# Kernel optimization log

Hardware: AMD Instinct MI355X
Metric: run time of the kernel (lower is better)

The kernel has to match this reference:

```python
import jax, jax.numpy as jnp
import numpy as np

B, CL, QL, D = 32, 1024, 512, 256


def setup_inputs() -> dict:
    key = jax.random.key(0)
    ks = jax.random.split(key, 8)
    c = jax.random.normal(ks[0], (B, CL, D), jnp.float32)
    q = jax.random.normal(ks[1], (B, QL, D), jnp.float32)
    scale = 1.0 / np.sqrt(D)
    w_c = jax.random.normal(ks[2], (D,), jnp.float32) * scale
    b_c = jax.random.normal(ks[3], (), jnp.float32) * 0.01
    w_q = jax.random.normal(ks[4], (D,), jnp.float32) * scale
    b_q = jax.random.normal(ks[5], (), jnp.float32) * 0.01
    w_cq = jax.random.normal(ks[6], (D,), jnp.float32) * scale
    b_cq = jax.random.normal(ks[7], (), jnp.float32) * 0.01
    return {"c": c, "q": q, "w_c": w_c, "b_c": b_c, "w_q": w_q, "b_q": b_q,
            "w_cq": w_cq, "b_cq": b_cq}


def reference(c, q, w_c, b_c, w_q, b_q, w_cq, b_cq):
    # s[b,i,j] = w_c.c_i + w_q.q_j + w_cq.(c_i*q_j) + biases
    sc = c @ w_c + b_c                                   # (B, CL)
    sq = q @ w_q + b_q                                   # (B, QL)
    # The original per-j loop att_weight_cq(c * q_j) is a batched bilinear form.
    cq = jnp.einsum('bid,bjd,d->bij', c, q, w_cq) + b_cq  # (B, CL, QL)
    s = sc[:, :, None] + sq[:, None, :] + cq              # (B, CL, QL)
    a = jax.nn.softmax(s, axis=2)
    c2q_att = jnp.einsum('bij,bjd->bid', a, q)            # (B, CL, D)
    bvec = jax.nn.softmax(jnp.max(s, axis=2), axis=1)     # (B, CL)
    q2c = jnp.einsum('bi,bid->bd', bvec, c)               # (B, D)
    q2c_att = jnp.broadcast_to(q2c[:, None, :], c.shape)  # (B, CL, D)
    x = jnp.concatenate([c, c2q_att, c * c2q_att, c * q2c_att], axis=-1)
    return x
```

## Files before the change

### kernel.cpp

```cpp
#include <hip/hip_runtime.h>

#define B_  32
#define CL_ 1024
#define QL_ 512
#define D_  256

typedef _Float16 f16;
typedef __attribute__((ext_vector_type(2))) _Float16 f16x2;
typedef __attribute__((ext_vector_type(4))) _Float16 f16x4;
typedef __attribute__((ext_vector_type(8))) _Float16 f16x8;
typedef __attribute__((ext_vector_type(4))) float    f32x4;

__global__ __launch_bounds__(256) void k0_prep(const float* __restrict__ q,
                                               const float* __restrict__ w_q,
                                               f16* __restrict__ qF,
                                               f16* __restrict__ qTF,
                                               float* __restrict__ sqv) {
  __shared__ f16 q_l[64][258];
  int b = blockIdx.y, J = blockIdx.x, j0 = J * 64, tid = threadIdx.x;
  int r = tid >> 2, seg = tid & 3;
  const float* qrow = q + ((size_t)(b * QL_ + j0 + r)) * D_ + seg * 64;
  float dot = 0.f;
  #pragma unroll
  for (int u = 0; u < 16; ++u) {
    f32x4 v  = *(const f32x4*)(qrow + 4 * u);
    f32x4 wv = *(const f32x4*)(w_q + seg * 64 + 4 * u);
    f16x4 h;
    h[0] = (f16)v[0]; h[1] = (f16)v[1]; h[2] = (f16)v[2]; h[3] = (f16)v[3];
    *(f16x4*)(&q_l[r][seg * 64 + 4 * u]) = h;
    dot += v[0]*wv[0] + v[1]*wv[1] + v[2]*wv[2] + v[3]*wv[3];
  }
  dot += __shfl_xor(dot, 1, 64);
  dot += __shfl_xor(dot, 2, 64);
  if (seg == 0) sqv[b * QL_ + j0 + r] = dot;
  __syncthreads();

  const int ww = tid >> 6, l = tid & 63, g = l >> 4, l15 = l & 15;
  f16* qFb = qF + ((size_t)(b * 8 + J)) * 16384;
  #pragma unroll
  for (int t = 0; t < 8; ++t) {
    int task = ww * 8 + t;
    int dk = task >> 2, fj = task & 3;
    f16x8 v = *(const f16x8*)(&q_l[16 * fj + l15][dk * 32 + 8 * g]);
    *(f16x8*)(qFb + ((size_t)task * 64 + l) * 8) = v;
  }
  #pragma unroll
  for (int t = 0; t < 8; ++t) {
    int task = ww * 8 + t;
    int W = task >> 2, jtl = (task >> 1) & 1, fd = task & 1;
    f16x8 v;
    #pragma unroll
    for (int e = 0; e < 8; ++e)
      v[e] = q_l[32 * jtl + 8 * g + e][32 * W + 16 * fd + l15];
    *(f16x8*)(qTF + ((((size_t)(b * 8 + W) * 16 + (2 * J + jtl)) * 2 + fd) * 64 + l) * 8) = v;
  }
}

__global__ __launch_bounds__(512, 2) void k1_fused(
    const float* __restrict__ c, const f16* __restrict__ qF,
    const f16* __restrict__ qTF, const float* __restrict__ sqv,
    const float* __restrict__ w_c, const float* __restrict__ w_cq,
    float* __restrict__ out, float* __restrict__ mrow)
{
  __shared__ alignas(16) char smem[142848];
  f16 (*cw_t)[264]  = (f16 (*)[264])(smem);
  char* P_b         = smem;
  float (*o_l)[260] = (float (*)[260])(smem);
  float* sqv_l = (float*)(smem + 133120);
  float* wcq_l = (float*)(smem + 135168);
  float* wc_l  = (float*)(smem + 136192);
  float* scv_l = (float*)(smem + 137216);
  float (*red)[128] = (float (*)[128])(smem + 137728);
  float* mf = (float*)(smem + 141824);
  float* lf = (float*)(smem + 142336);

  const int tid = threadIdx.x;
  const int w = tid >> 6, l = tid & 63, g = l >> 4, l15 = l & 15;
  const int lin = blockIdx.x, xcd = lin & 7, slot = lin >> 3;
  const int b  = xcd * 4 + (slot >> 3);
  const int i0 = (slot & 7) * 128;

  if (tid < 256) { wcq_l[tid] = w_cq[tid]; wc_l[tid] = w_c[tid]; }
  sqv_l[tid] = sqv[b * QL_ + tid];
  __syncthreads();

  {
    int row = tid >> 2, seg = tid & 3;
    const float* crow = c + (size_t)(b * CL_ + i0 + row) * D_ + seg * 64;
    float dot = 0.f;
    #pragma unroll
    for (int u = 0; u < 16; ++u) {
      f32x4 v  = *(const f32x4*)(crow + 4 * u);
      f32x4 wv = *(const f32x4*)(wcq_l + seg * 64 + 4 * u);
      f32x4 w2 = *(const f32x4*)(wc_l  + seg * 64 + 4 * u);
      f16x4 h;
      h[0] = (f16)(v[0]*wv[0]); h[1] = (f16)(v[1]*wv[1]);
      h[2] = (f16)(v[2]*wv[2]); h[3] = (f16)(v[3]*wv[3]);
      *(f16x4*)(&cw_t[row][seg * 64 + 4 * u]) = h;
      dot += v[0]*w2[0] + v[1]*w2[1] + v[2]*w2[2] + v[3]*w2[3];
    }
    dot += __shfl_xor(dot, 1, 64); dot += __shfl_xor(dot, 2, 64);
    if (seg == 0) scv_l[row] = dot;
  }
  __syncthreads();

  f32x4 acc[8][4];
  #pragma unroll
  for (int fi = 0; fi < 8; ++fi)
    #pragma unroll
    for (int fj = 0; fj < 4; ++fj)
      acc[fi][fj] = (f32x4){0.f,0.f,0.f,0.f};

  const f16* qFb = qF + ((size_t)(b * 8 + w)) * 16384;
  #pragma unroll
  for (int dk = 0; dk < 8; ++dk) {
    f16x8 av[8];
    #pragma unroll
    for (int fi = 0; fi < 8; ++fi)
      av[fi] = *(const f16x8*)(&cw_t[16 * fi + l15][dk * 32 + 8 * g]);
    #pragma unroll
    for (int fj = 0; fj < 4; ++fj) {
      f16x8 bf = *(const f16x8*)(qFb + (((size_t)dk * 4 + fj) * 64 + l) * 8);
      #pragma unroll
      for (int fi = 0; fi < 8; ++fi)
        acc[fi][fj] = __builtin_amdgcn_mfma_f32_16x16x32_f16(av[fi], bf, acc[fi][fj], 0, 0, 0);
    }
  }

  #pragma unroll
  for (int fi = 0; fi < 8; ++fi) {
    #pragma unroll
    for (int r = 0; r < 4; ++r) {
      float mx = -1e30f;
      #pragma unroll
      for (int fj = 0; fj < 4; ++fj) {
        float v = acc[fi][fj][r] + sqv_l[64 * w + 16 * fj + l15];
        acc[fi][fj][r] = v;
        mx = fmaxf(mx, v);
      }
      mx = fmaxf(mx, __shfl_xor(mx, 1, 64));
      mx = fmaxf(mx, __shfl_xor(mx, 2, 64));
      mx = fmaxf(mx, __shfl_xor(mx, 4, 64));
      mx = fmaxf(mx, __shfl_xor(mx, 8, 64));
      if (l15 == 0) red[w][16 * fi + 4 * g + r] = mx;
    }
  }
  __syncthreads();
  if (tid < 128) {
    float m = red[0][tid];
    #pragma unroll
    for (int w2 = 1; w2 < 8; ++w2) m = fmaxf(m, red[w2][tid]);
    mf[tid] = m;
    mrow[b * CL_ + i0 + tid] = m + scv_l[tid];
  }
  __syncthreads();
  #pragma unroll
  for (int fi = 0; fi < 8; ++fi) {
    #pragma unroll
    for (int r = 0; r < 4; ++r) {
      float mv = mf[16 * fi + 4 * g + r];
      float s = 0.f;
      #pragma unroll
      for (int fj = 0; fj < 4; ++fj) {
        float p = __expf(acc[fi][fj][r] - mv);
        acc[fi][fj][r] = p;
        s += p;
      }
      s += __shfl_xor(s, 1, 64); s += __shfl_xor(s, 2, 64);
      s += __shfl_xor(s, 4, 64); s += __shfl_xor(s, 8, 64);
      if (l15 == 0) red[w][16 * fi + 4 * g + r] = s;
    }
  }
  __syncthreads();
  if (tid < 128) {
    float s = 0.f;
    #pragma unroll
    for (int w2 = 0; w2 < 8; ++w2) s += red[w2][tid];
    lf[tid] = 1.0f / s;
  }
  __syncthreads();

  #pragma unroll
  for (int fi = 0; fi < 8; ++fi) {
    #pragma unroll
    for (int r = 0; r < 4; ++r) {
      int row = 16 * fi + 4 * g + r;
      float inv = lf[row];
      #pragma unroll
      for (int fj = 0; fj < 4; ++fj) {
        *(f16*)(P_b + (((row << 10) + 128 * w + 32 * fj + 2 * l15) ^ ((row & 7) << 4)))
            = (f16)(acc[fi][fj][r] * inv);
      }
    }
  }
  __syncthreads();

  f32x4 o[8][2];
  #pragma unroll
  for (int fi = 0; fi < 8; ++fi) { o[fi][0] = (f32x4){0.f,0.f,0.f,0.f}; o[fi][1] = o[fi][0]; }
  const f16* qTFb = qTF + ((size_t)(b * 8 + w)) * 16384;
  #pragma unroll
  for (int jt = 0; jt < 16; ++jt) {
    f16x8 qf0 = *(const f16x8*)(qTFb + (((size_t)jt * 2 + 0) * 64 + l) * 8);
    f16x8 qf1 = *(const f16x8*)(qTFb + (((size_t)jt * 2 + 1) * 64 + l) * 8);
    #pragma unroll
    for (int fi = 0; fi < 8; ++fi) {
      int row = 16 * fi + l15;
      f16x8 pa = *(const f16x8*)(P_b + (((row << 10) + 64 * jt + 16 * g) ^ ((row & 7) << 4)));
      o[fi][0] = __builtin_amdgcn_mfma_f32_16x16x32_f16(pa, qf0, o[fi][0], 0, 0, 0);
      o[fi][1] = __builtin_amdgcn_mfma_f32_16x16x32_f16(pa, qf1, o[fi][1], 0, 0, 0);
    }
  }
  __syncthreads();

  #pragma unroll
  for (int fi = 0; fi < 8; ++fi)
    #pragma unroll
    for (int fd = 0; fd < 2; ++fd)
      #pragma unroll
      for (int r = 0; r < 4; ++r)
        o_l[16 * fi + 4 * g + r][32 * w + 16 * fd + l15] = o[fi][fd][r];
  __syncthreads();

  #pragma unroll
  for (int s = 0; s < 16; ++s) {
    int idx = tid + 512 * s;
    int row = idx >> 6, c4 = (idx & 63) * 4;
    size_t rowoff = (size_t)(b * CL_ + i0 + row);
    f32x4 c2q = *(const f32x4*)(&o_l[row][c4]);
    f32x4 cv  = *(const f32x4*)(c + rowoff * D_ + c4);
    f32x4 prod;
    prod[0] = cv[0]*c2q[0]; prod[1] = cv[1]*c2q[1];
    prod[2] = cv[2]*c2q[2]; prod[3] = cv[3]*c2q[3];
    float* ob = out + rowoff * (4 * D_) + c4;
    *(f32x4*)(ob)          = cv;
    *(f32x4*)(ob + D_)     = c2q;
    *(f32x4*)(ob + 2 * D_) = prod;
  }
}

__global__ __launch_bounds__(256) void k2a_bvec(const float* __restrict__ mrow,
                                                float* __restrict__ bvec) {
  __shared__ float red[256];
  int b = blockIdx.x, tid = threadIdx.x;
  f32x4 v = *(const f32x4*)(mrow + b * CL_ + tid * 4);
  float mx = fmaxf(fmaxf(v[0], v[1]), fmaxf(v[2], v[3]));
  red[tid] = mx;
  __syncthreads();
  for (int s = 128; s > 0; s >>= 1) {
    if (tid < s) red[tid] = fmaxf(red[tid], red[tid + s]);
    __syncthreads();
  }
  float gmx = red[0];
  __syncthreads();
  f32x4 e;
  e[0] = __expf(v[0] - gmx); e[1] = __expf(v[1] - gmx);
  e[2] = __expf(v[2] - gmx); e[3] = __expf(v[3] - gmx);
  red[tid] = e[0] + e[1] + e[2] + e[3];
  __syncthreads();
  for (int s = 128; s > 0; s >>= 1) {
    if (tid < s) red[tid] += red[tid + s];
    __syncthreads();
  }
  float inv = 1.0f / red[0];
  e[0] *= inv; e[1] *= inv; e[2] *= inv; e[3] *= inv;
  *(f32x4*)(bvec + b * CL_ + tid * 4) = e;
}

__global__ __launch_bounds__(256) void k2b_part(const float* __restrict__ c,
                                                const float* __restrict__ bvec,
                                                float* __restrict__ part) {
  __shared__ f32x4 pl[4][64];
  int ch = blockIdx.x, b = blockIdx.y, tid = threadIdx.x;
  int ro = tid >> 6, dl = tid & 63;
  const float* cb = c + ((size_t)b * CL_ + ch * 128) * D_;
  const float* bv = bvec + b * CL_ + ch * 128;
  f32x4 acc = (f32x4){0.f, 0.f, 0.f, 0.f};
  for (int i = ro; i < 128; i += 4) {
    float wgt = bv[i];
    f32x4 v = *(const f32x4*)(cb + (size_t)i * D_ + dl * 4);
    acc[0] += wgt * v[0]; acc[1] += wgt * v[1];
    acc[2] += wgt * v[2]; acc[3] += wgt * v[3];
  }
  pl[ro][dl] = acc;
  __syncthreads();
  if (tid < 64) {
    f32x4 s = (pl[0][tid] + pl[1][tid]) + (pl[2][tid] + pl[3][tid]);
    *(f32x4*)(part + ((size_t)(b * 8 + ch)) * D_ + tid * 4) = s;
  }
}

__global__ __launch_bounds__(256) void k2c_red(const float* __restrict__ part,
                                               float* __restrict__ q2c) {
  int b = blockIdx.x, d = threadIdx.x;
  float s = 0.f;
  #pragma unroll
  for (int ch = 0; ch < 8; ++ch) s += part[((size_t)(b * 8 + ch)) * D_ + d];
  q2c[b * D_ + d] = s;
}

__global__ __launch_bounds__(256) void k3_tail(const float* __restrict__ c,
                                               const float* __restrict__ q2c,
                                               float* __restrict__ out) {
  size_t idx = (size_t)blockIdx.x * 256 + threadIdx.x;
  int b   = (int)(idx >> 16);
  int rem = (int)(idx & 65535);
  int i = rem >> 6, d4 = (rem & 63) * 4;
  f32x4 cv = *(const f32x4*)(c + (size_t)(b * CL_ + i) * D_ + d4);
  f32x4 gv = *(const f32x4*)(q2c + b * D_ + d4);
  f32x4 r;
  r[0] = cv[0]*gv[0]; r[1] = cv[1]*gv[1]; r[2] = cv[2]*gv[2]; r[3] = cv[3]*gv[3];
  *(f32x4*)(out + (size_t)(b * CL_ + i) * (4 * D_) + 3 * D_ + d4) = r;
}

extern "C" void kernel_launch(void* const* d_in, const int* in_sizes, int n_in,
                              void* d_out, int out_size, void* d_ws, size_t ws_size,
                              hipStream_t stream) {
  const float* c    = (const float*)d_in[0];
  const float* q    = (const float*)d_in[1];
  const float* w_c  = (const float*)d_in[2];
  const float* w_q  = (const float*)d_in[4];
  const float* w_cq = (const float*)d_in[6];
  float* out = (float*)d_out;
  char* ws = (char*)d_ws;
  f16*   qF   = (f16*)ws;
  f16*   qTF  = (f16*)(ws + 8388608);
  float* sqv  = (float*)(ws + 16777216);
  float* mrow = (float*)(ws + 16842752);
  float* bvec = (float*)(ws + 16973824);
  float* part = (float*)(ws + 17104896);
  float* q2c  = (float*)(ws + 17367040);

  hipLaunchKernelGGL(k0_prep,  dim3(8, 32),  dim3(256), 0, stream,
                     q, w_q, qF, qTF, sqv);
  hipLaunchKernelGGL(k1_fused, dim3(256),    dim3(512), 0, stream,
                     c, qF, qTF, sqv, w_c, w_cq, out, mrow);
  hipLaunchKernelGGL(k2a_bvec, dim3(32),     dim3(256), 0, stream, mrow, bvec);
  hipLaunchKernelGGL(k2b_part, dim3(8, 32),  dim3(256), 0, stream, c, bvec, part);
  hipLaunchKernelGGL(k2c_red,  dim3(32),     dim3(256), 0, stream, part, q2c);
  hipLaunchKernelGGL(k3_tail,  dim3(8192),   dim3(256), 0, stream, c, q2c, out);
}
```

Baseline: 95.09 us.

## Split c*w_cq prep into separate kernel and halve k1 row tile for occupancy

Moves the c*w_cq fp16 conversion and c·w_c dot product out of the fused attention kernel into a new prep kernel. That kernel writes MFMA-fragment-ordered fp16 data and scv to workspace. The fused kernel now processes 64 rows per block instead of 128, using about half the LDS and fewer accumulators, and launches 512 blocks with a higher occupancy hint. The aim is better latency hiding and more parallelism. The cost is an extra kernel launch, an extra global round trip for the cwF intermediate, and reloading q fragments twice as often across blocks.

```diff
diff --git a/kernel.cpp b/kernel.cpp
--- a/kernel.cpp
+++ b/kernel.cpp
@@ -56,79 +56,93 @@
   }
 }
 
-__global__ __launch_bounds__(512, 2) void k1_fused(
-    const float* __restrict__ c, const f16* __restrict__ qF,
+__global__ __launch_bounds__(256) void k0c_cw(const float* __restrict__ c,
+                                              const float* __restrict__ w_c,
+                                              const float* __restrict__ w_cq,
+                                              f16* __restrict__ cwF,
+                                              float* __restrict__ scv_ws) {
+  __shared__ f16 cw_l[64][264];
+  int T = blockIdx.x, b = blockIdx.y, tid = threadIdx.x;
+  int i0 = T * 64;
+  int row = tid >> 2, seg = tid & 3;
+  const float* crow = c + (size_t)(b * CL_ + i0 + row) * D_ + seg * 64;
+  float dot = 0.f;
+  #pragma unroll
+  for (int u = 0; u < 16; ++u) {
+    f32x4 v  = *(const f32x4*)(crow + 4 * u);
+    f32x4 wv = *(const f32x4*)(w_cq + seg * 64 + 4 * u);
+    f32x4 w2 = *(const f32x4*)(w_c  + seg * 64 + 4 * u);
+    f16x4 h;
+    h[0] = (f16)(v[0]*wv[0]); h[1] = (f16)(v[1]*wv[1]);
+    h[2] = (f16)(v[2]*wv[2]); h[3] = (f16)(v[3]*wv[3]);
+    *(f16x4*)(&cw_l[row][seg * 64 + 4 * u]) = h;
+    dot += v[0]*w2[0] + v[1]*w2[1] + v[2]*w2[2] + v[3]*w2[3];
+  }
+  dot += __shfl_xor(dot, 1, 64); dot += __shfl_xor(dot, 2, 64);
+  if (seg == 0) scv_ws[b * CL_ + i0 + row] = dot;
+  __syncthreads();
+
+  const int ww = tid >> 6, l = tid & 63, g = l >> 4, l15 = l & 15;
+  f16* dst = cwF + ((size_t)(b * 16 + T)) * 32 * 512;
+  #pragma unroll
+  for (int t = 0; t < 8; ++t) {
+    int task = ww * 8 + t;
+    int fi = task >> 3, dk = task & 7;
+    f16x8 v = *(const f16x8*)(&cw_l[16 * fi + l15][dk * 32 + 8 * g]);
+    *(f16x8*)(dst + ((size_t)task * 64 + l) * 8) = v;
+  }
+}
+
+__global__ __launch_bounds__(512, 4) void k1_fused(
+    const f16* __restrict__ cwF, const f16* __restrict__ qF,
     const f16* __restrict__ qTF, const float* __restrict__ sqv,
-    const float* __restrict__ w_c, const float* __restrict__ w_cq,
+    const float* __restrict__ scv_ws, const float* __restrict__ c,
     float* __restrict__ out, float* __restrict__ mrow)
 {
-  __shared__ alignas(16) char smem[142848];
-  f16 (*cw_t)[264]  = (f16 (*)[264])(smem);
-  char* P_b         = smem;
+  __shared__ alignas(16) char smem[71168];
+  f16 (*P_t)[520]   = (f16 (*)[520])(smem);
   float (*o_l)[260] = (float (*)[260])(smem);
-  float* sqv_l = (float*)(smem + 133120);
-  float* wcq_l = (float*)(smem + 135168);
-  float* wc_l  = (float*)(smem + 136192);
-  float* scv_l = (float*)(smem + 137216);
-  float (*red)[128] = (float (*)[128])(smem + 137728);
-  float* mf = (float*)(smem + 141824);
-  float* lf = (float*)(smem + 142336);
+  float* sqv_l = (float*)(smem + 66560);
+  float (*red)[64] = (float (*)[64])(smem + 68608);
+  float* mf = (float*)(smem + 70656);
+  float* lf = (float*)(smem + 70912);
 
   const int tid = threadIdx.x;
   const int w = tid >> 6, l = tid & 63, g = l >> 4, l15 = l & 15;
   const int lin = blockIdx.x, xcd = lin & 7, slot = lin >> 3;
-  const int b  = xcd * 4 + (slot >> 3);
-  const int i0 = (slot & 7) * 128;
-
-  if (tid < 256) { wcq_l[tid] = w_cq[tid]; wc_l[tid] = w_c[tid]; }
+  const int b  = xcd * 4 + (slot >> 4);
+  const int T  = slot & 15;
+  const int i0 = T * 64;
+
   sqv_l[tid] = sqv[b * QL_ + tid];
   __syncthreads();
 
-  {
-    int row = tid >> 2, seg = tid & 3;
-    const float* crow = c + (size_t)(b * CL_ + i0 + row) * D_ + seg * 64;
-    float dot = 0.f;
-    #pragma unroll
-    for (int u = 0; u < 16; ++u) {
-      f32x4 v  = *(const f32x4*)(crow + 4 * u);
-      f32x4 wv = *(const f32x4*)(wcq_l + seg * 64 + 4 * u);
-      f32x4 w2 = *(const f32x4*)(wc_l  + seg * 64 + 4 * u);
-      f16x4 h;
-      h[0] = (f16)(v[0]*wv[0]); h[1] = (f16)(v[1]*wv[1]);
-      h[2] = (f16)(v[2]*wv[2]); h[3] = (f16)(v[3]*wv[3]);
-      *(f16x4*)(&cw_t[row][seg * 64 + 4 * u]) = h;
-      dot += v[0]*w2[0] + v[1]*w2[1] + v[2]*w2[2] + v[3]*w2[3];
-    }
-    dot += __shfl_xor(dot, 1, 64); dot += __shfl_xor(dot, 2, 64);
-    if (seg == 0) scv_l[row] = dot;
-  }
-  __syncthreads();
-
-  f32x4 acc[8][4];
-  #pragma unroll
-  for (int fi = 0; fi < 8; ++fi)
+  f32x4 acc[4][4];
+  #pragma unroll
+  for (int fi = 0; fi < 4; ++fi)
     #pragma unroll
     for (int fj = 0; fj < 4; ++fj)
       acc[fi][fj] = (f32x4){0.f,0.f,0.f,0.f};
 
+  const f16* cwb = cwF + ((size_t)(b * 16 + T)) * 32 * 512;
   const f16* qFb = qF + ((size_t)(b * 8 + w)) * 16384;
   #pragma unroll
   for (int dk = 0; dk < 8; ++dk) {
-    f16x8 av[8];
-    #pragma unroll
-    for (int fi = 0; fi < 8; ++fi)
-      av[fi] = *(const f16x8*)(&cw_t[16 * fi + l15][dk * 32 + 8 * g]);
+    f16x8 av[4];
+    #pragma unroll
+    for (int fi = 0; fi < 4; ++fi)
+      av[fi] = *(const f16x8*)(cwb + (((size_t)fi * 8 + dk) * 64 + l) * 8);
     #pragma unroll
     for (int fj = 0; fj < 4; ++fj) {
       f16x8 bf = *(const f16x8*)(qFb + (((size_t)dk * 4 + fj) * 64 + l) * 8);
       #pragma unroll
-      for (int fi = 0; fi < 8; ++fi)
+      for (int fi = 0; fi < 4; ++fi)
         acc[fi][fj] = __builtin_amdgcn_mfma_f32_16x16x32_f16(av[fi], bf, acc[fi][fj], 0, 0, 0);
     }
   }
 
   #pragma unroll
-  for (int fi = 0; fi < 8; ++fi) {
+  for (int fi = 0; fi < 4; ++fi) {
     #pragma unroll
     for (int r = 0; r < 4; ++r) {
       float mx = -1e30f;
@@ -146,16 +160,16 @@
     }
   }
   __syncthreads();
-  if (tid < 128) {
+  if (tid < 64) {
     float m = red[0][tid];
     #pragma unroll
     for (int w2 = 1; w2 < 8; ++w2) m = fmaxf(m, red[w2][tid]);
     mf[tid] = m;
-    mrow[b * CL_ + i0 + tid] = m + scv_l[tid];
-  }
-  __syncthreads();
-  #pragma unroll
-  for (int fi = 0; fi < 8; ++fi) {
+    mrow[b * CL_ + i0 + tid] = m + scv_ws[b * CL_ + i0 + tid];
+  }
+  __syncthreads();
+  #pragma unroll
+  for (int fi = 0; fi < 4; ++fi) {
     #pragma unroll
     for (int r = 0; r < 4; ++r) {
       float mv = mf[16 * fi + 4 * g + r];
@@ -172,7 +186,7 @@
     }
   }
   __syncthreads();
-  if (tid < 128) {
+  if (tid < 64) {
     float s = 0.f;
     #pragma unroll
     for (int w2 = 0; w2 < 8; ++w2) s += red[w2][tid];
@@ -181,32 +195,29 @@
   __syncthreads();
 
   #pragma unroll
-  for (int fi = 0; fi < 8; ++fi) {
+  for (int fi = 0; fi < 4; ++fi) {
     #pragma unroll
     for (int r = 0; r < 4; ++r) {
       int row = 16 * fi + 4 * g + r;
       float inv = lf[row];
       #pragma unroll
-      for (int fj = 0; fj < 4; ++fj) {
-        *(f16*)(P_b + (((row << 10) + 128 * w + 32 * fj + 2 * l15) ^ ((row & 7) << 4)))
-            = (f16)(acc[fi][fj][r] * inv);
-      }
-    }
-  }
-  __syncthreads();
-
-  f32x4 o[8][2];
-  #pragma unroll
-  for (int fi = 0; fi < 8; ++fi) { o[fi][0] = (f32x4){0.f,0.f,0.f,0.f}; o[fi][1] = o[fi][0]; }
+      for (int fj = 0; fj < 4; ++fj)
+        P_t[row][64 * w + 16 * fj + l15] = (f16)(acc[fi][fj][r] * inv);
+    }
+  }
+  __syncthreads();
+
+  f32x4 o[4][2];
+  #pragma unroll
+  for (int fi = 0; fi < 4; ++fi) { o[fi][0] = (f32x4){0.f,0.f,0.f,0.f}; o[fi][1] = o[fi][0]; }
   const f16* qTFb = qTF + ((size_t)(b * 8 + w)) * 16384;
   #pragma unroll
   for (int jt = 0; jt < 16; ++jt) {
     f16x8 qf0 = *(const f16x8*)(qTFb + (((size_t)jt * 2 + 0) * 64 + l) * 8);
     f16x8 qf1 = *(const f16x8*)(qTFb + (((size_t)jt * 2 + 1) * 64 + l) * 8);
     #pragma unroll
-    for (int fi = 0; fi < 8; ++fi) {
-      int row = 16 * fi + l15;
-      f16x8 pa = *(const f16x8*)(P_b + (((row << 10) + 64 * jt + 16 * g) ^ ((row & 7) << 4)));
+    for (int fi = 0; fi < 4; ++fi) {
+      f16x8 pa = *(const f16x8*)(&P_t[16 * fi + l15][jt * 32 + 8 * g]);
       o[fi][0] = __builtin_amdgcn_mfma_f32_16x16x32_f16(pa, qf0, o[fi][0], 0, 0, 0);
       o[fi][1] = __builtin_amdgcn_mfma_f32_16x16x32_f16(pa, qf1, o[fi][1], 0, 0, 0);
     }
@@ -214,7 +225,7 @@
   __syncthreads();
 
   #pragma unroll
-  for (int fi = 0; fi < 8; ++fi)
+  for (int fi = 0; fi < 4; ++fi)
     #pragma unroll
     for (int fd = 0; fd < 2; ++fd)
       #pragma unroll
@@ -223,7 +234,7 @@
   __syncthreads();
 
   #pragma unroll
-  for (int s = 0; s < 16; ++s) {
+  for (int s = 0; s < 8; ++s) {
     int idx = tid + 512 * s;
     int row = idx >> 6, c4 = (idx & 63) * 4;
     size_t rowoff = (size_t)(b * CL_ + i0 + row);
@@ -323,20 +334,24 @@
   const float* w_cq = (const float*)d_in[6];
   float* out = (float*)d_out;
   char* ws = (char*)d_ws;
-  f16*   qF   = (f16*)ws;
-  f16*   qTF  = (f16*)(ws + 8388608);
-  float* sqv  = (float*)(ws + 16777216);
-  float* mrow = (float*)(ws + 16842752);
-  float* bvec = (float*)(ws + 16973824);
-  float* part = (float*)(ws + 17104896);
-  float* q2c  = (float*)(ws + 17367040);
-
-  hipLaunchKernelGGL(k0_prep,  dim3(8, 32),  dim3(256), 0, stream,
+  f16*   qF     = (f16*)ws;
+  f16*   qTF    = (f16*)(ws + 8388608);
+  f16*   cwF    = (f16*)(ws + 16777216);
+  float* sqv    = (float*)(ws + 33554432);
+  float* mrow   = (float*)(ws + 33619968);
+  float* bvec   = (float*)(ws + 33751040);
+  float* part   = (float*)(ws + 33882112);
+  float* q2c    = (float*)(ws + 34144256);
+  float* scv_ws = (float*)(ws + 34177024);
+
+  hipLaunchKernelGGL(k0_prep, dim3(8, 32),  dim3(256), 0, stream,
                      q, w_q, qF, qTF, sqv);
-  hipLaunchKernelGGL(k1_fused, dim3(256),    dim3(512), 0, stream,
-                     c, qF, qTF, sqv, w_c, w_cq, out, mrow);
-  hipLaunchKernelGGL(k2a_bvec, dim3(32),     dim3(256), 0, stream, mrow, bvec);
-  hipLaunchKernelGGL(k2b_part, dim3(8, 32),  dim3(256), 0, stream, c, bvec, part);
-  hipLaunchKernelGGL(k2c_red,  dim3(32),     dim3(256), 0, stream, part, q2c);
-  hipLaunchKernelGGL(k3_tail,  dim3(8192),   dim3(256), 0, stream, c, q2c, out);
-}
+  hipLaunchKernelGGL(k0c_cw,  dim3(16, 32), dim3(256), 0, stream,
+                     c, w_c, w_cq, cwF, scv_ws);
+  hipLaunchKernelGGL(k1_fused, dim3(512),   dim3(512), 0, stream,
+                     cwF, qF, qTF, sqv, scv_ws, c, out, mrow);
+  hipLaunchKernelGGL(k2a_bvec, dim3(32),    dim3(256), 0, stream, mrow, bvec);
+  hipLaunchKernelGGL(k2b_part, dim3(8, 32), dim3(256), 0, stream, c, bvec, part);
+  hipLaunchKernelGGL(k2c_red,  dim3(32),    dim3(256), 0, stream, part, q2c);
+  hipLaunchKernelGGL(k3_tail,  dim3(8192),  dim3(256), 0, stream, c, q2c, out);
+}
```

Measured after the change: 102.0 us. 7.3% more time.

## Move c2q output writes from fused attention kernel into a unified output kernel

Applied to the files above, without the earlier changes.

The fused attention kernel now stores only the c2q result as fp16 into a workspace buffer instead of writing three fp32 output slices. A new full-grid output kernel reads c, the fp16 c2q and q2c, and writes all four output slices. This pulls the heavy stores out of the low-occupancy MFMA kernel into a kernel that runs across the whole grid, at the cost of an extra fp16 round trip and added rounding of c2q.

```diff
diff --git a/kernel.cpp b/kernel.cpp
--- a/kernel.cpp
+++ b/kernel.cpp
@@ -60,12 +60,12 @@
     const float* __restrict__ c, const f16* __restrict__ qF,
     const f16* __restrict__ qTF, const float* __restrict__ sqv,
     const float* __restrict__ w_c, const float* __restrict__ w_cq,
-    float* __restrict__ out, float* __restrict__ mrow)
+    f16* __restrict__ c2qh, float* __restrict__ mrow)
 {
   __shared__ alignas(16) char smem[142848];
   f16 (*cw_t)[264]  = (f16 (*)[264])(smem);
   char* P_b         = smem;
-  float (*o_l)[260] = (float (*)[260])(smem);
+  f16 (*c2q_l)[264] = (f16 (*)[264])(smem);
   float* sqv_l = (float*)(smem + 133120);
   float* wcq_l = (float*)(smem + 135168);
   float* wc_l  = (float*)(smem + 136192);
@@ -219,23 +219,14 @@
     for (int fd = 0; fd < 2; ++fd)
       #pragma unroll
       for (int r = 0; r < 4; ++r)
-        o_l[16 * fi + 4 * g + r][32 * w + 16 * fd + l15] = o[fi][fd][r];
-  __syncthreads();
-
-  #pragma unroll
-  for (int s = 0; s < 16; ++s) {
+        c2q_l[16 * fi + 4 * g + r][32 * w + 16 * fd + l15] = (f16)o[fi][fd][r];
+  __syncthreads();
+  f16* dst = c2qh + ((size_t)(b * CL_ + i0)) * 256;
+  #pragma unroll
+  for (int s = 0; s < 8; ++s) {
     int idx = tid + 512 * s;
-    int row = idx >> 6, c4 = (idx & 63) * 4;
-    size_t rowoff = (size_t)(b * CL_ + i0 + row);
-    f32x4 c2q = *(const f32x4*)(&o_l[row][c4]);
-    f32x4 cv  = *(const f32x4*)(c + rowoff * D_ + c4);
-    f32x4 prod;
-    prod[0] = cv[0]*c2q[0]; prod[1] = cv[1]*c2q[1];
-    prod[2] = cv[2]*c2q[2]; prod[3] = cv[3]*c2q[3];
-    float* ob = out + rowoff * (4 * D_) + c4;
-    *(f32x4*)(ob)          = cv;
-    *(f32x4*)(ob + D_)     = c2q;
-    *(f32x4*)(ob + 2 * D_) = prod;
+    int row = idx >> 5, col8 = (idx & 31) * 8;
+    *(f16x8*)(dst + (size_t)row * 256 + col8) = *(const f16x8*)(&c2q_l[row][col8]);
   }
 }
 
@@ -299,18 +290,29 @@
   q2c[b * D_ + d] = s;
 }
 
-__global__ __launch_bounds__(256) void k3_tail(const float* __restrict__ c,
-                                               const float* __restrict__ q2c,
-                                               float* __restrict__ out) {
+__global__ __launch_bounds__(256) void k4_out(const float* __restrict__ c,
+                                              const f16* __restrict__ c2qh,
+                                              const float* __restrict__ q2c,
+                                              float* __restrict__ out) {
   size_t idx = (size_t)blockIdx.x * 256 + threadIdx.x;
   int b   = (int)(idx >> 16);
   int rem = (int)(idx & 65535);
   int i = rem >> 6, d4 = (rem & 63) * 4;
-  f32x4 cv = *(const f32x4*)(c + (size_t)(b * CL_ + i) * D_ + d4);
-  f32x4 gv = *(const f32x4*)(q2c + b * D_ + d4);
-  f32x4 r;
-  r[0] = cv[0]*gv[0]; r[1] = cv[1]*gv[1]; r[2] = cv[2]*gv[2]; r[3] = cv[3]*gv[3];
-  *(f32x4*)(out + (size_t)(b * CL_ + i) * (4 * D_) + 3 * D_ + d4) = r;
+  size_t rowoff = (size_t)(b * CL_ + i);
+  f32x4 cv = *(const f32x4*)(c + rowoff * D_ + d4);
+  f16x4 gh = *(const f16x4*)(c2qh + rowoff * 256 + d4);
+  f32x4 gv;
+  gv[0] = (float)gh[0]; gv[1] = (float)gh[1];
+  gv[2] = (float)gh[2]; gv[3] = (float)gh[3];
+  f32x4 qv = *(const f32x4*)(q2c + b * D_ + d4);
+  f32x4 p2, p3;
+  p2[0] = cv[0]*gv[0]; p2[1] = cv[1]*gv[1]; p2[2] = cv[2]*gv[2]; p2[3] = cv[3]*gv[3];
+  p3[0] = cv[0]*qv[0]; p3[1] = cv[1]*qv[1]; p3[2] = cv[2]*qv[2]; p3[3] = cv[3]*qv[3];
+  float* ob = out + rowoff * (4 * D_) + d4;
+  *(f32x4*)(ob)          = cv;
+  *(f32x4*)(ob + D_)     = gv;
+  *(f32x4*)(ob + 2 * D_) = p2;
+  *(f32x4*)(ob + 3 * D_) = p3;
 }
 
 extern "C" void kernel_launch(void* const* d_in, const int* in_sizes, int n_in,
@@ -330,13 +332,15 @@
   float* bvec = (float*)(ws + 16973824);
   float* part = (float*)(ws + 17104896);
   float* q2c  = (float*)(ws + 17367040);
+  f16*   c2qh = (f16*)(ws + 17399808);
 
   hipLaunchKernelGGL(k0_prep,  dim3(8, 32),  dim3(256), 0, stream,
                      q, w_q, qF, qTF, sqv);
   hipLaunchKernelGGL(k1_fused, dim3(256),    dim3(512), 0, stream,
-                     c, qF, qTF, sqv, w_c, w_cq, out, mrow);
+                     c, qF, qTF, sqv, w_c, w_cq, c2qh, mrow);
   hipLaunchKernelGGL(k2a_bvec, dim3(32),     dim3(256), 0, stream, mrow, bvec);
   hipLaunchKernelGGL(k2b_part, dim3(8, 32),  dim3(256), 0, stream, c, bvec, part);
   hipLaunchKernelGGL(k2c_red,  dim3(32),     dim3(256), 0, stream, part, q2c);
-  hipLaunchKernelGGL(k3_tail,  dim3(8192),   dim3(256), 0, stream, c, q2c, out);
-}
+  hipLaunchKernelGGL(k4_out,   dim3(8192),   dim3(256), 0, stream,
+                     c, c2qh, q2c, out);
+}
```

New measurement: 94.30 us. No clear change (-0.8%).
